# Optimization experiments

Measured on AMD Instinct MI355X. Metric: run time of the kernel, lower is better.

## Reference

```python
import jax, jax.numpy as jnp
import numpy as np

N = 100000
E = 1600000
D = 128
LAYERS = 2


def setup_inputs() -> dict:
    key = jax.random.key(0)
    k1, k2, k3, k4, k5, k6 = jax.random.split(key, 6)
    features = jax.random.normal(k1, (N, D), dtype=jnp.float32)
    edge_row = jax.random.randint(k2, (E,), 0, N)
    edge_col = jax.random.randint(k3, (E,), 0, N)
    edge_val = jax.random.uniform(k4, (E,), dtype=jnp.float32)
    # new_features[index] = out_features with out_features having N rows =>
    # index is a permutation covering all N nodes
    index = jax.random.permutation(k5, N)
    a_in = jax.random.normal(k6, (3,), dtype=jnp.float32)
    return {"features": features, "edge_row": edge_row, "edge_col": edge_col,
            "edge_val": edge_val, "index": index, "a_in": a_in}


def reference(features, edge_row, edge_col, edge_val, index, a_in):
    n, d = features.shape
    # --- normalize_adj: D^{-1/2} A D^{-1/2} (Mat is constant across layers) ---
    rowsum = jax.ops.segment_sum(edge_val, edge_row, num_segments=n)  # [N]
    d_inv_sqrt = jnp.where(rowsum > 0, rowsum ** -0.5, 0.0)
    vals = d_inv_sqrt[edge_row] * edge_val * d_inv_sqrt[edge_col]      # [E]

    # softmax over first Layers+1 entries of a_in
    a = jax.nn.softmax(a_in[:LAYERS + 1])

    # nodes covered by index keep the SpMM result; others keep old features
    covered = jnp.zeros((n,), dtype=bool).at[index].set(True)

    result = a[0] * features
    h = features
    for j in range(LAYERS):
        # SpMM: out[r] = sum_e vals[e] * h[col[e]] for row[e] == r
        out = jax.ops.segment_sum(vals[:, None] * h[edge_col], edge_row,
                                  num_segments=n)                      # [N, D]
        scattered = jnp.zeros_like(h).at[index].set(out)
        h = jnp.where(covered[:, None], scattered, h)
        result = result + a[j + 1] * h
    return result
```

## Files before the change

### kernel.cpp

```cpp
#include <hip/hip_runtime.h>

#define WPB    4
#define SCAN_B 1024
#define P1B    256
#define BKT_SH 8

typedef unsigned u32x4 __attribute__((ext_vector_type(4)));
typedef float    f32x4 __attribute__((ext_vector_type(4)));
typedef float    f32x2 __attribute__((ext_vector_type(2)));

__device__ __forceinline__ unsigned bf16rne(float x) {
  unsigned u = __float_as_uint(x);
  return (u + 0x7fffu + ((u >> 16) & 1u)) >> 16;
}
__device__ __forceinline__ float bf_lo(unsigned g) { return __uint_as_float(g << 16); }
__device__ __forceinline__ float bf_hi(unsigned g) { return __uint_as_float(g & 0xffff0000u); }

__global__ void prep_p1_k(const f32x2* __restrict__ f, unsigned* __restrict__ hb, int nw,
                          const float* __restrict__ a_in, float* __restrict__ a_buf,
                          const int* __restrict__ index, int* __restrict__ covered,
                          int* __restrict__ row_start, const int* __restrict__ erow,
                          int* __restrict__ bhist, int E, int N, int C, int NB) {
  extern __shared__ int h[];
  const bool dop1 = (blockIdx.x < P1B);
  if (dop1) {
    for (int k = threadIdx.x; k < NB; k += 256) h[k] = 0;
    __syncthreads();
  }
  int i = blockIdx.x * 256 + threadIdx.x;
  if (i < nw) {
    f32x2 v = __builtin_nontemporal_load(f + i);
    hb[i] = bf16rne(v.x) | (bf16rne(v.y) << 16);
  }
  if (i < N) covered[index[i]] = 1;
  if (i == 0) {
    row_start[N] = E;
    float x0 = a_in[0], x1 = a_in[1], x2 = a_in[2];
    float m = fmaxf(x0, fmaxf(x1, x2));
    float e0 = expf(x0 - m), e1 = expf(x1 - m), e2 = expf(x2 - m);
    float s = e0 + e1 + e2;
    a_buf[0] = e0 / s; a_buf[1] = e1 / s; a_buf[2] = e2 / s;
  }
  if (dop1) {
    int s = blockIdx.x * C, e = min(E, s + C);
    for (int j = s + threadIdx.x; j < e; j += 256)
      atomicAdd(&h[erow[j] >> BKT_SH], 1);
    __syncthreads();
    for (int k = threadIdx.x; k < NB; k += 256)
      bhist[(size_t)k * P1B + blockIdx.x] = h[k];
  }
}

__global__ void scanA_k(const int* __restrict__ cnt, int* __restrict__ incl,
                        int* __restrict__ bsum, int n) {
  __shared__ int tmp[SCAN_B];
  int tid = threadIdx.x;
  int g = blockIdx.x * SCAN_B + tid;
  tmp[tid] = (g < n) ? cnt[g] : 0;
  __syncthreads();
  for (int off = 1; off < SCAN_B; off <<= 1) {
    int t = (tid >= off) ? tmp[tid - off] : 0;
    __syncthreads();
    tmp[tid] += t;
    __syncthreads();
  }
  if (g < n) incl[g] = tmp[tid];
  if (tid == SCAN_B - 1) bsum[blockIdx.x] = tmp[tid];
}

__global__ void scanBC_k(int* __restrict__ boffs, const int* __restrict__ bhist,
                         const int* __restrict__ bsum, int nb, int n) {
  __shared__ int bs[128];
  int tid = threadIdx.x;
  if (tid < 128) bs[tid] = (tid < nb) ? bsum[tid] : 0;
  __syncthreads();
  for (int off = 1; off < 128; off <<= 1) {
    int t = (tid >= off && tid < 128) ? bs[tid - off] : 0;
    __syncthreads();
    if (tid < 128) bs[tid] += t;
    __syncthreads();
  }
  int g = blockIdx.x * SCAN_B + tid;
  if (g < n) {
    int off2 = (blockIdx.x > 0) ? bs[blockIdx.x - 1] : 0;
    boffs[g] = boffs[g] + off2 - bhist[g];
  }
}

__global__ void p2_k(const int* __restrict__ row, const int* __restrict__ col,
                     const float* __restrict__ val, const int* __restrict__ boffs,
                     int2* __restrict__ bedge, int E, int C, int NB) {
  extern __shared__ int cur[];
  for (int k = threadIdx.x; k < NB; k += 256)
    cur[k] = boffs[(size_t)k * P1B + blockIdx.x];
  __syncthreads();
  int s = blockIdx.x * C, e = min(E, s + C);
  for (int i = s + threadIdx.x; i < e; i += 256) {
    int r = row[i];
    int p = atomicAdd(&cur[r >> BKT_SH], 1);
    bedge[p] = make_int2(((r & 255) << 24) | col[i], __float_as_int(val[i]));
  }
}

__global__ void p3_k(const int2* __restrict__ bedge, const int* __restrict__ boffs,
                     int* __restrict__ row_start, float* __restrict__ dis,
                     int2* __restrict__ pairs, int E, int N, int NB) {
  __shared__ int rcnt[256];
  __shared__ float rsum[256];
  __shared__ int rbase[256];
  __shared__ int tmp[256];
  int kb = blockIdx.x, t = threadIdx.x;
  int base = boffs[(size_t)kb * P1B];
  int end  = (kb + 1 < NB) ? boffs[(size_t)(kb + 1) * P1B] : E;
  rcnt[t] = 0; rsum[t] = 0.f;
  __syncthreads();
  for (int i = base + t; i < end; i += 256) {
    int2 p = bedge[i];
    int rlo = ((unsigned)p.x) >> 24;
    atomicAdd(&rcnt[rlo], 1);
    atomicAdd(&rsum[rlo], __int_as_float(p.y));
  }
  __syncthreads();
  int v = rcnt[t];
  tmp[t] = v;
  __syncthreads();
  for (int off = 1; off < 256; off <<= 1) {
    int u = (t >= off) ? tmp[t - off] : 0;
    __syncthreads();
    tmp[t] += u;
    __syncthreads();
  }
  rbase[t] = tmp[t] - v;
  int r = (kb << BKT_SH) + t;
  if (r < N) {
    row_start[r] = base + rbase[t];
    float s = rsum[t];
    dis[r] = (s > 0.0f) ? rsqrtf(s) : 0.0f;
  }
  __syncthreads();
  rcnt[t] = rbase[t];
  __syncthreads();
  for (int i = base + t; i < end; i += 256) {
    int2 p = bedge[i];
    int rlo = ((unsigned)p.x) >> 24;
    int pos = base + atomicAdd(&rcnt[rlo], 1);
    pairs[pos] = make_int2(p.x & 0xFFFFFF, p.y);
  }
}

__global__ void scale_k(int2* __restrict__ pairs, const float* __restrict__ dis, int E) {
  int i = blockIdx.x * 256 + threadIdx.x;
  if (i < E) {
    int2 p = pairs[i];
    p.y = __float_as_int(__int_as_float(p.y) * dis[p.x]);
    pairs[i] = p;
  }
}

__device__ __forceinline__ void acc8(float v, u32x4 g, float* a) {
  a[0] = fmaf(v, bf_lo(g.x), a[0]); a[1] = fmaf(v, bf_hi(g.x), a[1]);
  a[2] = fmaf(v, bf_lo(g.y), a[2]); a[3] = fmaf(v, bf_hi(g.y), a[3]);
  a[4] = fmaf(v, bf_lo(g.z), a[4]); a[5] = fmaf(v, bf_hi(g.z), a[5]);
  a[6] = fmaf(v, bf_lo(g.w), a[6]); a[7] = fmaf(v, bf_hi(g.w), a[7]);
}

__device__ __forceinline__ void spmm_body(const int* __restrict__ row_start,
                                          const int2* __restrict__ pairs,
                                          const char* __restrict__ hb,
                                          int wave, int lane, float* a) {
  int q = lane >> 4;
  unsigned qoff = (unsigned)(lane & 15) << 4;
  int beg = row_start[wave], end = row_start[wave + 1];
  for (int base = beg; base < end; base += 64) {
    unsigned long long pl = 0;
    if (base + lane < end)
      pl = __builtin_nontemporal_load((const unsigned long long*)(pairs + base + lane));
    int pc = (int)(pl & 0xffffffffu);
    float pv = __uint_as_float((unsigned)(pl >> 32));
    int m = end - base; if (m > 64) m = 64;
    for (int j = 0; j < m; j += 16) {
      int   c0 = __shfl(pc, j + q),      c1 = __shfl(pc, j + 4 + q);
      int   c2 = __shfl(pc, j + 8 + q),  c3 = __shfl(pc, j + 12 + q);
      float v0 = __shfl(pv, j + q),      v1 = __shfl(pv, j + 4 + q);
      float v2 = __shfl(pv, j + 8 + q),  v3 = __shfl(pv, j + 12 + q);
      u32x4 g0 = *(const u32x4*)(hb + (((unsigned)c0 << 8) | qoff));
      u32x4 g1 = *(const u32x4*)(hb + (((unsigned)c1 << 8) | qoff));
      u32x4 g2 = *(const u32x4*)(hb + (((unsigned)c2 << 8) | qoff));
      u32x4 g3 = *(const u32x4*)(hb + (((unsigned)c3 << 8) | qoff));
      acc8(v0, g0, a); acc8(v1, g1, a);
      acc8(v2, g2, a); acc8(v3, g3, a);
    }
  }
#pragma unroll
  for (int i = 0; i < 8; ++i) a[i] += __shfl_xor(a[i], 16);
#pragma unroll
  for (int i = 0; i < 8; ++i) a[i] += __shfl_xor(a[i], 32);
}

__global__ void spmm1_k(const int* __restrict__ row_start, const int2* __restrict__ pairs,
                        const float* __restrict__ dis, const unsigned* __restrict__ hB,
                        const int* __restrict__ index, u32x4* __restrict__ hA4, int n) {
  int wave = blockIdx.x * WPB + (threadIdx.x >> 6);
  if (wave >= n) return;
  int lane = threadIdx.x & 63;
  float a[8] = {0.f, 0.f, 0.f, 0.f, 0.f, 0.f, 0.f, 0.f};
  spmm_body(row_start, pairs, (const char*)hB, wave, lane, a);
  if ((lane >> 4) == 0) {
    float dr = dis[wave];
    u32x4 pk;
    pk.x = bf16rne(a[0] * dr) | (bf16rne(a[1] * dr) << 16);
    pk.y = bf16rne(a[2] * dr) | (bf16rne(a[3] * dr) << 16);
    pk.z = bf16rne(a[4] * dr) | (bf16rne(a[5] * dr) << 16);
    pk.w = bf16rne(a[6] * dr) | (bf16rne(a[7] * dr) << 16);
    hA4[(unsigned)index[wave] * 16u + (unsigned)(lane & 15)] = pk;
  }
}

__global__ void spmm2_k(const int* __restrict__ row_start, const int2* __restrict__ pairs,
                        const float* __restrict__ dis, const u32x4* __restrict__ hA4,
                        const u32x4* __restrict__ hB4, const int* __restrict__ index,
                        f32x4* __restrict__ out4, const float* __restrict__ ac, int n) {
  int wave = blockIdx.x * WPB + (threadIdx.x >> 6);
  if (wave >= n) return;
  int lane = threadIdx.x & 63;
  float a[8] = {0.f, 0.f, 0.f, 0.f, 0.f, 0.f, 0.f, 0.f};
  spmm_body(row_start, pairs, (const char*)hA4, wave, lane, a);
  if ((lane >> 4) == 0) {
    unsigned ql = lane & 15;
    float dr = dis[wave];
    unsigned ro = (unsigned)index[wave] * 16u + ql;
    u32x4 ga = hA4[ro];
    u32x4 gb = __builtin_nontemporal_load(hB4 + ro);
    float c0 = ac[0], c1 = ac[1], c2 = ac[2];
    f32x4 w0, w1;
    w0.x = fmaf(c2, a[0] * dr, fmaf(c1, bf_lo(ga.x), c0 * bf_lo(gb.x)));
    w0.y = fmaf(c2, a[1] * dr, fmaf(c1, bf_hi(ga.x), c0 * bf_hi(gb.x)));
    w0.z = fmaf(c2, a[2] * dr, fmaf(c1, bf_lo(ga.y), c0 * bf_lo(gb.y)));
    w0.w = fmaf(c2, a[3] * dr, fmaf(c1, bf_hi(ga.y), c0 * bf_hi(gb.y)));
    w1.x = fmaf(c2, a[4] * dr, fmaf(c1, bf_lo(ga.z), c0 * bf_lo(gb.z)));
    w1.y = fmaf(c2, a[5] * dr, fmaf(c1, bf_hi(ga.z), c0 * bf_hi(gb.z)));
    w1.z = fmaf(c2, a[6] * dr, fmaf(c1, bf_lo(ga.w), c0 * bf_lo(gb.w)));
    w1.w = fmaf(c2, a[7] * dr, fmaf(c1, bf_hi(ga.w), c0 * bf_hi(gb.w)));
    unsigned ob = (unsigned)index[wave] * 32u + 2u * ql;
    __builtin_nontemporal_store(w0, out4 + ob);
    __builtin_nontemporal_store(w1, out4 + ob + 1);
  }
}

__global__ void fixup1_k(const int* __restrict__ covered, const u32x4* __restrict__ hB4,
                         u32x4* __restrict__ hA4, int n) {
  int v = blockIdx.x * 256 + threadIdx.x;
  if (v >= n || covered[v]) return;
  for (int d = 0; d < 16; ++d) hA4[(size_t)v * 16 + d] = hB4[(size_t)v * 16 + d];
}

__global__ void fixup2_k(const int* __restrict__ covered, const float2* __restrict__ feat,
                         float2* __restrict__ out, const float* __restrict__ a, int n) {
  int v = blockIdx.x * 256 + threadIdx.x;
  if (v >= n || covered[v]) return;
  float s = a[0] + a[1] + a[2];
  for (int d = 0; d < 64; ++d) {
    float2 f = feat[(size_t)v * 64 + d];
    out[(size_t)v * 64 + d] = make_float2(s * f.x, s * f.y);
  }
}

extern "C" void kernel_launch(void* const* d_in, const int* in_sizes, int n_in,
                              void* d_out, int out_size, void* d_ws, size_t ws_size,
                              hipStream_t stream) {
  const float* features = (const float*)d_in[0];
  const int*   edge_row = (const int*)d_in[1];
  const int*   edge_col = (const int*)d_in[2];
  const float* edge_val = (const float*)d_in[3];
  const int*   index    = (const int*)d_in[4];
  const float* a_in     = (const float*)d_in[5];

  const int E = in_sizes[1];
  const int N = in_sizes[4];
  const int NB = (N + 255) >> BKT_SH;
  const int NBH = NB * P1B;
  const int C = (E + P1B - 1) / P1B;

  float* out = (float*)d_out;

  char* ws = (char*)d_ws;
  size_t off = 0;
  auto carve = [&](size_t bytes) -> char* {
    char* p = ws + off;
    off = (off + bytes + 255) & ~(size_t)255;
    return p;
  };
  float* a_buf     = (float*)carve(16 * sizeof(float));
  float* dis       = (float*)carve((size_t)N * 4);
  int*   covered   = (int*)carve((size_t)N * 4);
  int*   row_start = (int*)carve((size_t)(N + 1) * 4);
  int*   bsum      = (int*)carve(256 * 4);
  int2*  pairs     = (int2*)carve((size_t)E * 8);
  unsigned* hB     = (unsigned*)carve((size_t)N * 64 * 4);
  size_t ov_bytes = (size_t)NBH * 4 * 2 + (size_t)E * 8 + 1024;
  size_t hA_bytes = (size_t)N * 64 * 4;
  char* ovl = carve(ov_bytes > hA_bytes ? ov_bytes : hA_bytes);
  int*  bhist = (int*)ovl;
  int*  boffs = (int*)(ovl + (((size_t)NBH * 4 + 255) & ~(size_t)255));
  int2* bedge = (int2*)(ovl + 2 * (((size_t)NBH * 4 + 255) & ~(size_t)255));
  unsigned* hA = (unsigned*)ovl;
  (void)ws_size; (void)n_in; (void)out_size;

  const int nbE = (E + 255) / 256;
  const int nbW = (N * 64 + 255) / 256;
  const int nbScan = (NBH + SCAN_B - 1) / SCAN_B;
  const int nbN = (N + 255) / 256;
  const size_t ldsB = (size_t)NB * 4;

  hipMemsetAsync(covered, 0, (size_t)N * 4, stream);
  prep_p1_k<<<nbW, 256, ldsB, stream>>>((const f32x2*)features, hB, N * 64,
                                        a_in, a_buf, index, covered, row_start,
                                        edge_row, bhist, E, N, C, NB);
  scanA_k<<<nbScan, SCAN_B, 0, stream>>>(bhist, boffs, bsum, NBH);
  scanBC_k<<<nbScan, SCAN_B, 0, stream>>>(boffs, bhist, bsum, nbScan, NBH);
  p2_k<<<P1B, 256, ldsB, stream>>>(edge_row, edge_col, edge_val, boffs, bedge, E, C, NB);
  p3_k<<<NB, 256, 0, stream>>>(bedge, boffs, row_start, dis, pairs, E, N, NB);
  scale_k<<<nbE, 256, 0, stream>>>(pairs, dis, E);

  const int nbSpmm = (N + WPB - 1) / WPB;
  spmm1_k<<<nbSpmm, WPB * 64, 0, stream>>>(row_start, pairs, dis, hB, index,
                                           (u32x4*)hA, N);
  fixup1_k<<<nbN, 256, 0, stream>>>(covered, (const u32x4*)hB, (u32x4*)hA, N);
  spmm2_k<<<nbSpmm, WPB * 64, 0, stream>>>(row_start, pairs, dis, (const u32x4*)hA,
                                           (const u32x4*)hB, index, (f32x4*)out,
                                           a_buf, N);
  fixup2_k<<<nbN, 256, 0, stream>>>(covered, (const float2*)features,
                                    (float2*)out, a_buf, N);
}
```

Measured before the change: 213.3 us.

## Split SpMM feature dimension across XCD halves and fuse fixups into SpMM

Each SpMM row is now processed by two waves, each covering half of the 128 feature columns. Block indices are mapped so that blocks on XCDs 0-3 handle one half and blocks on XCDs 4-7 the other, so each XCD's L2 caches only half of the gathered feature rows. The uncovered-node fixup passes are folded into the tail of the SpMM kernels, and the covered-flag init moves into prep and p2, which removes a memset and two launches. The cost is twice as many waves re-reading row_start and the edge pairs, plus a dependence on the round-robin block-to-XCD assignment.

```diff
diff --git a/kernel.cpp b/kernel.cpp
--- a/kernel.cpp
+++ b/kernel.cpp
@@ -5,6 +5,7 @@
 #define P1B    256
 #define BKT_SH 8
 
+typedef unsigned u32x2 __attribute__((ext_vector_type(2)));
 typedef unsigned u32x4 __attribute__((ext_vector_type(4)));
 typedef float    f32x4 __attribute__((ext_vector_type(4)));
 typedef float    f32x2 __attribute__((ext_vector_type(2)));
@@ -18,9 +19,9 @@
 
 __global__ void prep_p1_k(const f32x2* __restrict__ f, unsigned* __restrict__ hb, int nw,
                           const float* __restrict__ a_in, float* __restrict__ a_buf,
-                          const int* __restrict__ index, int* __restrict__ covered,
-                          int* __restrict__ row_start, const int* __restrict__ erow,
-                          int* __restrict__ bhist, int E, int N, int C, int NB) {
+                          int* __restrict__ covered, int* __restrict__ row_start,
+                          const int* __restrict__ erow, int* __restrict__ bhist,
+                          int E, int N, int C, int NB) {
   extern __shared__ int h[];
   const bool dop1 = (blockIdx.x < P1B);
   if (dop1) {
@@ -32,7 +33,7 @@
     f32x2 v = __builtin_nontemporal_load(f + i);
     hb[i] = bf16rne(v.x) | (bf16rne(v.y) << 16);
   }
-  if (i < N) covered[index[i]] = 1;
+  if (i < N) covered[i] = 0;
   if (i == 0) {
     row_start[N] = E;
     float x0 = a_in[0], x1 = a_in[1], x2 = a_in[2];
@@ -89,11 +90,14 @@
 
 __global__ void p2_k(const int* __restrict__ row, const int* __restrict__ col,
                      const float* __restrict__ val, const int* __restrict__ boffs,
-                     int2* __restrict__ bedge, int E, int C, int NB) {
+                     int2* __restrict__ bedge, const int* __restrict__ index,
+                     int* __restrict__ covered, int E, int N, int C, int NB) {
   extern __shared__ int cur[];
   for (int k = threadIdx.x; k < NB; k += 256)
     cur[k] = boffs[(size_t)k * P1B + blockIdx.x];
   __syncthreads();
+  for (int i = blockIdx.x * 256 + threadIdx.x; i < N; i += P1B * 256)
+    covered[index[i]] = 1;
   int s = blockIdx.x * C, e = min(E, s + C);
   for (int i = s + threadIdx.x; i < e; i += 256) {
     int r = row[i];
@@ -157,20 +161,18 @@
   }
 }
 
-__device__ __forceinline__ void acc8(float v, u32x4 g, float* a) {
+__device__ __forceinline__ void acc4(float v, u32x2 g, float* a) {
   a[0] = fmaf(v, bf_lo(g.x), a[0]); a[1] = fmaf(v, bf_hi(g.x), a[1]);
   a[2] = fmaf(v, bf_lo(g.y), a[2]); a[3] = fmaf(v, bf_hi(g.y), a[3]);
-  a[4] = fmaf(v, bf_lo(g.z), a[4]); a[5] = fmaf(v, bf_hi(g.z), a[5]);
-  a[6] = fmaf(v, bf_lo(g.w), a[6]); a[7] = fmaf(v, bf_hi(g.w), a[7]);
-}
-
-__device__ __forceinline__ void spmm_body(const int* __restrict__ row_start,
-                                          const int2* __restrict__ pairs,
-                                          const char* __restrict__ hb,
-                                          int wave, int lane, float* a) {
+}
+
+__device__ __forceinline__ void spmm_body_h(const int* __restrict__ row_start,
+                                            const int2* __restrict__ pairs,
+                                            const char* __restrict__ hb,
+                                            int row, int lane, unsigned hoff, float* a) {
   int q = lane >> 4;
-  unsigned qoff = (unsigned)(lane & 15) << 4;
-  int beg = row_start[wave], end = row_start[wave + 1];
+  unsigned qoff = ((unsigned)(lane & 15) << 3) | hoff;
+  int beg = row_start[row], end = row_start[row + 1];
   for (int base = beg; base < end; base += 64) {
     unsigned long long pl = 0;
     if (base + lane < end)
@@ -183,85 +185,89 @@
       int   c2 = __shfl(pc, j + 8 + q),  c3 = __shfl(pc, j + 12 + q);
       float v0 = __shfl(pv, j + q),      v1 = __shfl(pv, j + 4 + q);
       float v2 = __shfl(pv, j + 8 + q),  v3 = __shfl(pv, j + 12 + q);
-      u32x4 g0 = *(const u32x4*)(hb + (((unsigned)c0 << 8) | qoff));
-      u32x4 g1 = *(const u32x4*)(hb + (((unsigned)c1 << 8) | qoff));
-      u32x4 g2 = *(const u32x4*)(hb + (((unsigned)c2 << 8) | qoff));
-      u32x4 g3 = *(const u32x4*)(hb + (((unsigned)c3 << 8) | qoff));
-      acc8(v0, g0, a); acc8(v1, g1, a);
-      acc8(v2, g2, a); acc8(v3, g3, a);
+      u32x2 g0 = *(const u32x2*)(hb + (((unsigned)c0 << 8) | qoff));
+      u32x2 g1 = *(const u32x2*)(hb + (((unsigned)c1 << 8) | qoff));
+      u32x2 g2 = *(const u32x2*)(hb + (((unsigned)c2 << 8) | qoff));
+      u32x2 g3 = *(const u32x2*)(hb + (((unsigned)c3 << 8) | qoff));
+      acc4(v0, g0, a); acc4(v1, g1, a);
+      acc4(v2, g2, a); acc4(v3, g3, a);
     }
   }
 #pragma unroll
-  for (int i = 0; i < 8; ++i) a[i] += __shfl_xor(a[i], 16);
+  for (int i = 0; i < 4; ++i) a[i] += __shfl_xor(a[i], 16);
 #pragma unroll
-  for (int i = 0; i < 8; ++i) a[i] += __shfl_xor(a[i], 32);
+  for (int i = 0; i < 4; ++i) a[i] += __shfl_xor(a[i], 32);
 }
 
 __global__ void spmm1_k(const int* __restrict__ row_start, const int2* __restrict__ pairs,
                         const float* __restrict__ dis, const unsigned* __restrict__ hB,
-                        const int* __restrict__ index, u32x4* __restrict__ hA4, int n) {
-  int wave = blockIdx.x * WPB + (threadIdx.x >> 6);
-  if (wave >= n) return;
+                        const int* __restrict__ index, const int* __restrict__ covered,
+                        u32x2* __restrict__ hA2, int n) {
+  int xcd = blockIdx.x & 7;
+  unsigned hoff = (unsigned)(xcd >> 2) << 7;
+  int rb = (blockIdx.x >> 3) * 4 + (xcd & 3);
+  int wave = rb * WPB + (threadIdx.x >> 6);
   int lane = threadIdx.x & 63;
-  float a[8] = {0.f, 0.f, 0.f, 0.f, 0.f, 0.f, 0.f, 0.f};
-  spmm_body(row_start, pairs, (const char*)hB, wave, lane, a);
-  if ((lane >> 4) == 0) {
-    float dr = dis[wave];
-    u32x4 pk;
-    pk.x = bf16rne(a[0] * dr) | (bf16rne(a[1] * dr) << 16);
-    pk.y = bf16rne(a[2] * dr) | (bf16rne(a[3] * dr) << 16);
-    pk.z = bf16rne(a[4] * dr) | (bf16rne(a[5] * dr) << 16);
-    pk.w = bf16rne(a[6] * dr) | (bf16rne(a[7] * dr) << 16);
-    hA4[(unsigned)index[wave] * 16u + (unsigned)(lane & 15)] = pk;
+  if (wave < n) {
+    float a[4] = {0.f, 0.f, 0.f, 0.f};
+    spmm_body_h(row_start, pairs, (const char*)hB, wave, lane, hoff, a);
+    if (lane < 16) {
+      float dr = dis[wave];
+      u32x2 pk;
+      pk.x = bf16rne(a[0] * dr) | (bf16rne(a[1] * dr) << 16);
+      pk.y = bf16rne(a[2] * dr) | (bf16rne(a[3] * dr) << 16);
+      hA2[(unsigned)index[wave] * 32u + (hoff >> 3) + (unsigned)lane] = pk;
+    }
+  }
+  int gtid = blockIdx.x * 256 + threadIdx.x;
+  int stride = gridDim.x * 256;
+  const u32x4* s4 = (const u32x4*)hB;
+  u32x4* d4 = (u32x4*)hA2;
+  for (int v = gtid; v < n; v += stride) {
+    if (!covered[v]) {
+      for (int d = 0; d < 16; ++d) d4[(size_t)v * 16 + d] = s4[(size_t)v * 16 + d];
+    }
   }
 }
 
 __global__ void spmm2_k(const int* __restrict__ row_start, const int2* __restrict__ pairs,
-                        const float* __restrict__ dis, const u32x4* __restrict__ hA4,
-                        const u32x4* __restrict__ hB4, const int* __restrict__ index,
+                        const float* __restrict__ dis, const u32x2* __restrict__ hA2,
+                        const u32x2* __restrict__ hB2, const int* __restrict__ index,
+                        const int* __restrict__ covered, const f32x4* __restrict__ feat4,
                         f32x4* __restrict__ out4, const float* __restrict__ ac, int n) {
-  int wave = blockIdx.x * WPB + (threadIdx.x >> 6);
-  if (wave >= n) return;
+  int xcd = blockIdx.x & 7;
+  unsigned hoff = (unsigned)(xcd >> 2) << 7;
+  int rb = (blockIdx.x >> 3) * 4 + (xcd & 3);
+  int wave = rb * WPB + (threadIdx.x >> 6);
   int lane = threadIdx.x & 63;
-  float a[8] = {0.f, 0.f, 0.f, 0.f, 0.f, 0.f, 0.f, 0.f};
-  spmm_body(row_start, pairs, (const char*)hA4, wave, lane, a);
-  if ((lane >> 4) == 0) {
-    unsigned ql = lane & 15;
-    float dr = dis[wave];
-    unsigned ro = (unsigned)index[wave] * 16u + ql;
-    u32x4 ga = hA4[ro];
-    u32x4 gb = __builtin_nontemporal_load(hB4 + ro);
-    float c0 = ac[0], c1 = ac[1], c2 = ac[2];
-    f32x4 w0, w1;
-    w0.x = fmaf(c2, a[0] * dr, fmaf(c1, bf_lo(ga.x), c0 * bf_lo(gb.x)));
-    w0.y = fmaf(c2, a[1] * dr, fmaf(c1, bf_hi(ga.x), c0 * bf_hi(gb.x)));
-    w0.z = fmaf(c2, a[2] * dr, fmaf(c1, bf_lo(ga.y), c0 * bf_lo(gb.y)));
-    w0.w = fmaf(c2, a[3] * dr, fmaf(c1, bf_hi(ga.y), c0 * bf_hi(gb.y)));
-    w1.x = fmaf(c2, a[4] * dr, fmaf(c1, bf_lo(ga.z), c0 * bf_lo(gb.z)));
-    w1.y = fmaf(c2, a[5] * dr, fmaf(c1, bf_hi(ga.z), c0 * bf_hi(gb.z)));
-    w1.z = fmaf(c2, a[6] * dr, fmaf(c1, bf_lo(ga.w), c0 * bf_lo(gb.w)));
-    w1.w = fmaf(c2, a[7] * dr, fmaf(c1, bf_hi(ga.w), c0 * bf_hi(gb.w)));
-    unsigned ob = (unsigned)index[wave] * 32u + 2u * ql;
-    __builtin_nontemporal_store(w0, out4 + ob);
-    __builtin_nontemporal_store(w1, out4 + ob + 1);
-  }
-}
-
-__global__ void fixup1_k(const int* __restrict__ covered, const u32x4* __restrict__ hB4,
-                         u32x4* __restrict__ hA4, int n) {
-  int v = blockIdx.x * 256 + threadIdx.x;
-  if (v >= n || covered[v]) return;
-  for (int d = 0; d < 16; ++d) hA4[(size_t)v * 16 + d] = hB4[(size_t)v * 16 + d];
-}
-
-__global__ void fixup2_k(const int* __restrict__ covered, const float2* __restrict__ feat,
-                         float2* __restrict__ out, const float* __restrict__ a, int n) {
-  int v = blockIdx.x * 256 + threadIdx.x;
-  if (v >= n || covered[v]) return;
-  float s = a[0] + a[1] + a[2];
-  for (int d = 0; d < 64; ++d) {
-    float2 f = feat[(size_t)v * 64 + d];
-    out[(size_t)v * 64 + d] = make_float2(s * f.x, s * f.y);
+  if (wave < n) {
+    float a[4] = {0.f, 0.f, 0.f, 0.f};
+    spmm_body_h(row_start, pairs, (const char*)hA2, wave, lane, hoff, a);
+    if (lane < 16) {
+      float dr = dis[wave];
+      unsigned ro = (unsigned)index[wave] * 32u + (hoff >> 3) + (unsigned)lane;
+      u32x2 ga = hA2[ro];
+      u32x2 gb = __builtin_nontemporal_load(hB2 + ro);
+      float c0 = ac[0], c1 = ac[1], c2 = ac[2];
+      f32x4 w;
+      w.x = fmaf(c2, a[0] * dr, fmaf(c1, bf_lo(ga.x), c0 * bf_lo(gb.x)));
+      w.y = fmaf(c2, a[1] * dr, fmaf(c1, bf_hi(ga.x), c0 * bf_hi(gb.x)));
+      w.z = fmaf(c2, a[2] * dr, fmaf(c1, bf_lo(ga.y), c0 * bf_lo(gb.y)));
+      w.w = fmaf(c2, a[3] * dr, fmaf(c1, bf_hi(ga.y), c0 * bf_hi(gb.y)));
+      __builtin_nontemporal_store(w, out4 + ro);
+    }
+  }
+  int gtid = blockIdx.x * 256 + threadIdx.x;
+  int stride = gridDim.x * 256;
+  for (int v = gtid; v < n; v += stride) {
+    if (!covered[v]) {
+      float s = ac[0] + ac[1] + ac[2];
+      for (int d = 0; d < 32; ++d) {
+        f32x4 f = feat4[(size_t)v * 32 + d];
+        f32x4 w; w.x = s * f.x; w.y = s * f.y; w.z = s * f.z; w.w = s * f.w;
+        out4[(size_t)v * 32 + d] = w;
+      }
+    }
   }
 }
 
@@ -309,26 +315,23 @@
   const int nbE = (E + 255) / 256;
   const int nbW = (N * 64 + 255) / 256;
   const int nbScan = (NBH + SCAN_B - 1) / SCAN_B;
-  const int nbN = (N + 255) / 256;
   const size_t ldsB = (size_t)NB * 4;
 
-  hipMemsetAsync(covered, 0, (size_t)N * 4, stream);
   prep_p1_k<<<nbW, 256, ldsB, stream>>>((const f32x2*)features, hB, N * 64,
-                                        a_in, a_buf, index, covered, row_start,
+                                        a_in, a_buf, covered, row_start,
                                         edge_row, bhist, E, N, C, NB);
   scanA_k<<<nbScan, SCAN_B, 0, stream>>>(bhist, boffs, bsum, NBH);
   scanBC_k<<<nbScan, SCAN_B, 0, stream>>>(boffs, bhist, bsum, nbScan, NBH);
-  p2_k<<<P1B, 256, ldsB, stream>>>(edge_row, edge_col, edge_val, boffs, bedge, E, C, NB);
+  p2_k<<<P1B, 256, ldsB, stream>>>(edge_row, edge_col, edge_val, boffs, bedge,
+                                   index, covered, E, N, C, NB);
   p3_k<<<NB, 256, 0, stream>>>(bedge, boffs, row_start, dis, pairs, E, N, NB);
   scale_k<<<nbE, 256, 0, stream>>>(pairs, dis, E);
 
-  const int nbSpmm = (N + WPB - 1) / WPB;
-  spmm1_k<<<nbSpmm, WPB * 64, 0, stream>>>(row_start, pairs, dis, hB, index,
-                                           (u32x4*)hA, N);
-  fixup1_k<<<nbN, 256, 0, stream>>>(covered, (const u32x4*)hB, (u32x4*)hA, N);
-  spmm2_k<<<nbSpmm, WPB * 64, 0, stream>>>(row_start, pairs, dis, (const u32x4*)hA,
-                                           (const u32x4*)hB, index, (f32x4*)out,
-                                           a_buf, N);
-  fixup2_k<<<nbN, 256, 0, stream>>>(covered, (const float2*)features,
-                                    (float2*)out, a_buf, N);
-}
+  const int nbRB = (N + WPB - 1) / WPB;
+  const int grid = ((nbRB + 3) / 4) * 8;
+  spmm1_k<<<grid, 256, 0, stream>>>(row_start, pairs, dis, hB, index, covered,
+                                    (u32x2*)hA, N);
+  spmm2_k<<<grid, 256, 0, stream>>>(row_start, pairs, dis, (const u32x2*)hA,
+                                    (const u32x2*)hB, index, covered,
+                                    (const f32x4*)features, (f32x4*)out, a_buf, N);
+}
```

New measurement: 314.2 us. 1.47x slower.
